# Kernel tuning notes

Hardware: AMD Instinct MI355X
Metric: run time of the kernel (lower is better)

The kernel has to match this reference:

```python
import jax, jax.numpy as jnp
import numpy as np


def _conv1x1(x, w, b):
    # x: (B,Ci,H,W), w: (Co,Ci) -> (B,Co,H,W)
    return jnp.einsum('bchw,oc->bohw', x, w) + b[None, :, None, None]


def _conv3x3(x, w, b):
    # x: (B,Ci,H,W), w: (Co,Ci,3,3), stride 1, padding 1 ('SAME')
    y = jax.lax.conv_general_dilated(
        x, w, window_strides=(1, 1), padding='SAME',
        dimension_numbers=('NCHW', 'OIHW', 'NCHW'))
    return y + b[None, :, None, None]


def setup_inputs() -> dict:
    key = jax.random.key(0)
    ks = jax.random.split(key, 10)
    N, B, Cc, Cf, H, W = 3, 8, 128, 256, 64, 64
    s = 0.05  # weight scale to keep attention logits well-conditioned
    return {
        'contexts': jax.random.normal(ks[0], (N, B, Cc, 2 * H, 2 * W), jnp.float32),
        'mainstream': jax.random.normal(ks[1], (B, Cf, H, W), jnp.float32),
        'Wc_w': jax.random.normal(ks[2], (Cc, Cc), jnp.float32) * s,
        'Wc_b': jax.random.normal(ks[3], (Cc,), jnp.float32) * s,
        'Wf_w': jax.random.normal(ks[4], (Cc, Cf), jnp.float32) * s,
        'Wf_b': jax.random.normal(ks[5], (Cc,), jnp.float32) * s,
        'Wk_w': jax.random.normal(ks[6], (Cc, Cf), jnp.float32) * s,
        'Wk_b': jax.random.normal(ks[7], (Cc,), jnp.float32) * s,
        'Wv_w': jax.random.normal(ks[8], (Cc, Cf, 3, 3), jnp.float32) * s,
        'Wv_b': jax.random.normal(ks[9], (Cc,), jnp.float32) * s,
    }


def reference(contexts, mainstream, Wc_w, Wc_b, Wf_w, Wf_b, Wk_w, Wk_b, Wv_w, Wv_b):
    N, B, Cc = contexts.shape[0], contexts.shape[1], contexts.shape[2]
    H, W = mainstream.shape[2], mainstream.shape[3]

    q = _conv1x1(mainstream, Wf_w, Wf_b)        # (B,Cc,H,W) queries
    mkey = _conv1x1(mainstream, Wk_w, Wk_b)     # (B,Cc,H,W) mainline keys
    vals = _conv3x3(mainstream, Wv_w, Wv_b)     # (B,Cc,H,W) mainline values
    ckeys = jax.vmap(lambda c: _conv1x1(c, Wc_w, Wc_b))(contexts)  # (N,B,Cc,2H,2W)

    # unfold 2x2 sub-pixel blocks: (.., 2H, 2W) -> (.., H, 2, W, 2)
    ckeys = ckeys.reshape(N, B, Cc, H, 2, W, 2)
    cfeat = contexts.reshape(N, B, Cc, H, 2, W, 2)

    # per-pixel cross-attention logits: context keys . query
    logits_ctx = jnp.einsum('nbchiwj,bchw->nbhiwj', ckeys, q)      # (N,B,H,2,W,2)
    # mainline key . query (same logit for all 4 sub-pixels)
    logit_main = jnp.einsum('bchw,bchw->bhw', mkey, q)[None, :, :, None, :, None]
    logits = jnp.concatenate(
        [logits_ctx, jnp.broadcast_to(logit_main, (1, B, H, 2, W, 2))], axis=0)

    attn = jax.nn.softmax(logits, axis=0)                          # (N+1,B,H,2,W,2)

    vfeat = jnp.broadcast_to(vals[None, :, :, :, None, :, None],
                             (1, B, Cc, H, 2, W, 2))
    feats = jnp.concatenate([cfeat, vfeat], axis=0)                # (N+1,B,Cc,H,2,W,2)

    out = jnp.einsum('nbhiwj,nbchiwj->bchiwj', attn, feats)        # (B,Cc,H,2,W,2)
    return out.reshape(B, Cc, 2 * H, 2 * W)
```

## Files before the change

### kernel.cpp

```cpp
#include <hip/hip_runtime.h>

#define NCTX 3
#define B 8
#define CC 128
#define CF 256
#define H 64
#define W 64
#define HW 4096
#define YX 16384

#define WS_QT    0
#define WS_VALS  4194304
#define WS_BIAS  8388608
#define WS_LM    8421376
#define WS_WALL  8454144
#define WS_MSP   8552960
#define WS_WB    13013504
#define WS_WALLO 13160960

typedef __attribute__((ext_vector_type(8))) short bf16x8;
typedef __attribute__((ext_vector_type(4))) float f32x4;
typedef __attribute__((ext_vector_type(8))) unsigned short u16x8;

__device__ __forceinline__ unsigned short f2b(float f) {
    union { float f; unsigned u; } c; c.f = f;
    unsigned u = c.u + 0x7FFFu + ((c.u >> 16) & 1u);
    return (unsigned short)(u >> 16);
}
__device__ __forceinline__ float b2f(unsigned short u) {
    union { unsigned u; float f; } c; c.u = ((unsigned)u) << 16;
    return c.f;
}

__global__ void k0(const float* __restrict__ Wc_w, const float* __restrict__ Wc_b,
                   const float* __restrict__ Wf_w, const float* __restrict__ Wf_b,
                   const float* __restrict__ Wk_w, const float* __restrict__ Wk_b,
                   const float* __restrict__ Wv,
                   unsigned short* __restrict__ Wall, unsigned short* __restrict__ Wallo,
                   float* __restrict__ bias448, unsigned short* __restrict__ Wb,
                   unsigned short* __restrict__ msP) {
    int blk = blockIdx.x;
    int t = threadIdx.x;
    if (blk < 448) {
        int o = blk * 256 + t;
        int ci8 = o & 7;
        int idx = o >> 3;
        int row = idx % 448;
        int sc4 = idx / 448;
        int f = (sc4 >> 2) * 32 + (sc4 & 3) * 8 + ci8;
        float w;
        if (row < 128) {
            float s = 0.f;
            for (int o2 = 0; o2 < 128; ++o2) s += Wc_w[o2 * 128 + row] * Wf_w[o2 * 256 + f];
            w = s;
        } else if (row < 384) {
            int p = (row - 128) >> 1;
            w = (row & 1) ? Wk_w[p * 256 + f] : Wf_w[p * 256 + f];
        } else if (row == 384) {
            float s = 0.f;
            for (int o2 = 0; o2 < 128; ++o2) s += Wc_b[o2] * Wf_w[o2 * 256 + f];
            w = s;
        } else w = 0.f;
        unsigned short hi = f2b(w);
        Wall[o] = hi;
        Wallo[o] = f2b(w - b2f(hi));
        if (o < 448) {
            float bb;
            if (o < 128) {
                float s = 0.f;
                for (int o2 = 0; o2 < 128; ++o2) s += Wc_w[o2 * 128 + o] * Wf_b[o2];
                bb = s;
            } else if (o < 384) {
                int p = (o - 128) >> 1;
                bb = (o & 1) ? Wk_b[p] : Wf_b[p];
            } else if (o == 384) {
                float s = 0.f;
                for (int o2 = 0; o2 < 128; ++o2) s += Wc_b[o2] * Wf_b[o2];
                bb = s;
            } else if (o == 385) bb = -1.f;
            else bb = 0.f;
            bias448[o] = bb;
        }
    } else if (blk < 1600) {
        int o = (blk - 448) * 256 + t;
        int ci8 = o & 7;
        int co  = (o >> 3) & 127;
        int c4  = (o >> 10) & 3;
        int s   = (o >> 12) & 7;
        int khw = o >> 15;
        int ci  = s * 32 + c4 * 8 + ci8;
        int kh  = khw / 3, kw = khw - kh * 3;
        Wb[o] = f2b(Wv[((co * 256 + ci) * 3 + kh) * 3 + kw]);
    } else {
        int i = (blk - 1600) * 256 + t;
        if (i < 66560) {
            size_t off;
            if (i < 33792) {
                int x = i % 66; int r = i / 66;
                int g = r & 31, rowi = (r >> 5) & 1, b = r >> 6;
                off = ((((size_t)b * 66 + rowi * 65) * 32) + g) * 66 + x;
            } else {
                int k = i - 33792;
                int xi = k & 1; int g = (k >> 1) & 31; int y1 = (k >> 6) & 63; int b = k >> 12;
                off = ((((size_t)b * 66 + (y1 + 1)) * 32) + g) * 66 + xi * 65;
            }
            *(u16x8*)&msP[off * 8] = (u16x8){0, 0, 0, 0, 0, 0, 0, 0};
        }
    }
}

__global__ __launch_bounds__(256) void k2p(const float* __restrict__ ms,
                                           unsigned short* __restrict__ msP,
                                           unsigned short* __restrict__ msLo) {
    __shared__ float Ls[32][65];
    int t = threadIdx.x;
    int blk = blockIdx.x;
    int s = blk & 7;
    int h = (blk >> 3) & 63;
    int b = blk >> 9;
    const float* src = ms + ((size_t)b * 256 + s * 32) * HW + h * 64;
    for (int l = t; l < 2048; l += 256) {
        int ci = l >> 6, w = l & 63;
        Ls[ci][w] = src[ci * HW + w];
    }
    __syncthreads();
    int w = t & 63, gi = t >> 6;
    u16x8 vh, vl;
#pragma unroll
    for (int j = 0; j < 8; ++j) {
        float f = Ls[gi * 8 + j][w];
        unsigned short hb = f2b(f);
        vh[j] = hb;
        vl[j] = f2b(f - b2f(hb));
    }
    size_t offH = ((((size_t)b * 66 + (h + 1)) * 32) + (s * 4 + gi)) * 66 + (w + 1);
    *(u16x8*)&msP[offH * 8] = vh;
    size_t offL = ((((size_t)b * 64 + h) * 32) + (s * 4 + gi)) * 64 + w;
    *(u16x8*)&msLo[offL * 8] = vl;
}

__global__ __launch_bounds__(512, 4) void k1m(const unsigned short* __restrict__ msP,
                                              const unsigned short* __restrict__ msLo,
                                              const unsigned short* __restrict__ Wall,
                                              const unsigned short* __restrict__ Wallo,
                                              const float* __restrict__ bias448,
                                              float* __restrict__ qt, float* __restrict__ lm) {
    __shared__ unsigned short Bs[2][2][4][64][8];
    __shared__ float biasS[448];
    __shared__ float lmAcc[64];
    int t = threadIdx.x;
    int lane = t & 63, wid = t >> 6;
    int wm = wid >> 1, wn = wid & 1;
    int b = blockIdx.x >> 6, h = blockIdx.x & 63;
    int c4l = lane >> 4, lrow = lane & 15;
    for (int i = t; i < 448; i += 512) biasS[i] = bias448[i];
    if (t < 64) lmAcc[t] = 0.f;

    f32x4 acc[7][2];
#pragma unroll
    for (int mf = 0; mf < 7; ++mf)
#pragma unroll
        for (int nf = 0; nf < 2; ++nf) acc[mf][nf] = (f32x4){0.f, 0.f, 0.f, 0.f};

    const bf16x8* Whip = (const bf16x8*)Wall;
    const bf16x8* Wlop = (const bf16x8*)Wallo;

#define STAGE1(bufv, sv) do {                                                       \
    int pl_ = wid >> 2, c4_ = wid & 3;                                              \
    if (pl_ == 0) {                                                                 \
        const unsigned short* gph = msP +                                           \
            (((((size_t)b * 66 + (h + 1)) * 32) + ((sv) * 4 + c4_)) * 66            \
             + (lane + 1)) * 8;                                                     \
        __builtin_amdgcn_global_load_lds(                                           \
            (const __attribute__((address_space(1))) void*)gph,                     \
            (__attribute__((address_space(3))) void*)&Bs[bufv][0][c4_][0][0],       \
            16, 0, 0);                                                              \
    } else {                                                                        \
        const unsigned short* gpl = msLo +                                          \
            (((((size_t)b * 64 + h) * 32) + ((sv) * 4 + c4_)) * 64 + lane) * 8;     \
        __builtin_amdgcn_global_load_lds(                                           \
            (const __attribute__((address_space(1))) void*)gpl,                     \
            (__attribute__((address_space(3))) void*)&Bs[bufv][1][c4_][0][0],       \
            16, 0, 0);                                                              \
    }                                                                               \
} while (0)

    STAGE1(0, 0);
    __syncthreads();

    for (int s = 0; s < 8; ++s) {
        int cur = s & 1;
        if (s < 7) STAGE1(cur ^ 1, s + 1);
        bf16x8 bh[2], bl[2];
#pragma unroll
        for (int nf = 0; nf < 2; ++nf) {
            int x = wn * 32 + nf * 16 + lrow;
            bh[nf] = *(const bf16x8*)&Bs[cur][0][c4l][x][0];
            bl[nf] = *(const bf16x8*)&Bs[cur][1][c4l][x][0];
        }
#pragma unroll
        for (int mf = 0; mf < 7; ++mf) {
            size_t widx = (size_t)(s * 4 + c4l) * 448 + wm * 112 + mf * 16 + lrow;
            bf16x8 ah = Whip[widx];
            bf16x8 al = Wlop[widx];
#pragma unroll
            for (int nf = 0; nf < 2; ++nf) {
                acc[mf][nf] = __builtin_amdgcn_mfma_f32_16x16x32_bf16(ah, bh[nf], acc[mf][nf], 0, 0, 0);
                acc[mf][nf] = __builtin_amdgcn_mfma_f32_16x16x32_bf16(ah, bl[nf], acc[mf][nf], 0, 0, 0);
                acc[mf][nf] = __builtin_amdgcn_mfma_f32_16x16x32_bf16(al, bh[nf], acc[mf][nf], 0, 0, 0);
            }
        }
        __syncthreads();
    }

    int px0 = wn * 32;
    float lmp[2] = {0.f, 0.f};
#pragma unroll
    for (int mf = 0; mf < 7; ++mf) {
        int base = wm * 112 + mf * 16;
        int r0 = base + c4l * 4;
        if (base < 128) {
#pragma unroll
            for (int nf = 0; nf < 2; ++nf) {
                int x = px0 + nf * 16 + lrow;
                float* dst = qt + ((size_t)b * 128 + r0) * HW + h * 64 + x;
                f32x4 v = acc[mf][nf];
#pragma unroll
                for (int j = 0; j < 4; ++j)
                    dst[(size_t)j * HW] = v[j] + biasS[r0 + j];
            }
        } else {
            float b0 = biasS[r0], b1 = biasS[r0 + 1], b2 = biasS[r0 + 2], b3 = biasS[r0 + 3];
#pragma unroll
            for (int nf = 0; nf < 2; ++nf) {
                f32x4 v = acc[mf][nf];
                lmp[nf] += (v[0] + b0) * (v[1] + b1) + (v[2] + b2) * (v[3] + b3);
            }
        }
    }
    if (wm != 0) {
#pragma unroll
        for (int nf = 0; nf < 2; ++nf) {
            lmp[nf] += __shfl_xor(lmp[nf], 16);
            lmp[nf] += __shfl_xor(lmp[nf], 32);
        }
        if (c4l == 0) {
#pragma unroll
            for (int nf = 0; nf < 2; ++nf)
                atomicAdd(&lmAcc[px0 + nf * 16 + lrow], lmp[nf]);
        }
    }
    __syncthreads();
    if (t < 64) lm[b * HW + h * 64 + t] = lmAcc[t];
#undef STAGE1
}

__global__ __launch_bounds__(256, 4) void k2m(const unsigned short* __restrict__ msP,
                                              const unsigned short* __restrict__ Wb,
                                              const float* __restrict__ Wv_b,
                                              float* __restrict__ vals) {
    __shared__ unsigned short Bs[2][6336];
    __shared__ float biasS[128];
    int t = threadIdx.x;
    int lane = t & 63, wid = t >> 6;
    int wm = wid;
    int b = blockIdx.x >> 6, h = blockIdx.x & 63;
    int c4l = lane >> 4, lrow = lane & 15;
    if (t < 128) biasS[t] = Wv_b[t];

    f32x4 acc[2][4];
#pragma unroll
    for (int mf = 0; mf < 2; ++mf)
#pragma unroll
        for (int nf = 0; nf < 4; ++nf) acc[mf][nf] = (f32x4){0.f, 0.f, 0.f, 0.f};

    const bf16x8* Wbp = (const bf16x8*)Wb;

#define STAGE(bufv, sv) do {                                                        \
    for (int iter = 0; iter < 4; ++iter) {                                          \
        int q0 = iter * 256 + (wid << 6);                                           \
        int q = q0 + lane;                                                          \
        if (q < 792) {                                                              \
            int rc = q / 66; int x = q - rc * 66;                                   \
            int r = rc >> 2, c4 = rc & 3;                                           \
            int y = h + r;                                   \
            const unsigned short* gp = msP +                                        \
                (((((size_t)b * 66 + y) * 32) + ((sv) * 4 + c4)) * 66 + x) * 8;     \
            unsigned short* lp = &Bs[bufv][q0 * 8];                                 \
            __builtin_amdgcn_global_load_lds(                                       \
                (const __attribute__((address_space(1))) void*)gp,                  \
                (__attribute__((address_space(3))) void*)lp, 16, 0, 0);             \
        }                                                                           \
    }                                                                               \
} while (0)

    STAGE(0, 0);
    __syncthreads();

    for (int s = 0; s < 8; ++s) {
        int cur = s & 1;
        if (s < 7) STAGE(cur ^ 1, s + 1);
#pragma unroll
        for (int khw = 0; khw < 9; ++khw) {
            int kh = khw / 3, kw = khw - 3 * (khw / 3);
            bf16x8 a[2];
#pragma unroll
            for (int mf = 0; mf < 2; ++mf)
                a[mf] = Wbp[((khw * 8 + s) * 4 + c4l) * 128 + wm * 32 + mf * 16 + lrow];
            bf16x8 bf[4];
#pragma unroll
            for (int nf = 0; nf < 4; ++nf) {
                int chunk = (kh * 4 + c4l) * 66 + nf * 16 + lrow + kw;
                bf[nf] = *(const bf16x8*)&Bs[cur][chunk * 8];
            }
#pragma unroll
            for (int mf = 0; mf < 2; ++mf)
#pragma unroll
                for (int nf = 0; nf < 4; ++nf)
                    acc[mf][nf] = __builtin_amdgcn_mfma_f32_16x16x32_bf16(
                        a[mf], bf[nf], acc[mf][nf], 0, 0, 0);
        }
        __syncthreads();
    }

#pragma unroll
    for (int mf = 0; mf < 2; ++mf) {
        int co0 = wm * 32 + mf * 16 + c4l * 4;
#pragma unroll
        for (int nf = 0; nf < 4; ++nf) {
            int x = nf * 16 + lrow;
            float* dst = vals + (((size_t)b * 128 + co0) * HW) + h * 64 + x;
            f32x4 v = acc[mf][nf];
#pragma unroll
            for (int j = 0; j < 4; ++j)
                dst[(size_t)j * HW] = v[j] + biasS[co0 + j];
        }
    }
#undef STAGE
}

__global__ __launch_bounds__(256, 2) void k3(
    const float* __restrict__ ctx, const float* __restrict__ qt,
    const float* __restrict__ vals, const float* __restrict__ lm,
    float* __restrict__ out) {
    __shared__ float part[4][3][64];
    __shared__ float attnS[4][64];
    int t = threadIdx.x;
    int lane = t & 63, wv = t >> 6;
    int xg = t & 15, cq = t >> 4;
    int blk = blockIdx.x;
    int b = blk >> 8, y = (blk >> 1) & 127, xh = blk & 1;
    int h = y >> 1;
    int x0 = xh * 64 + xg * 4;
    int p0 = xh * 32 + xg * 2;

    float2 qv[8], vv[8];
    const float* qbase = qt + ((size_t)b * 128 + cq * 8) * HW + h * 64 + p0;
    const float* vbase = vals + ((size_t)b * 128 + cq * 8) * HW + h * 64 + p0;
#pragma unroll
    for (int j = 0; j < 8; ++j) {
        qv[j] = *(const float2*)&qbase[(size_t)j * HW];
        vv[j] = *(const float2*)&vbase[(size_t)j * HW];
    }
    float4 cx[3][8];
#pragma unroll
    for (int n = 0; n < 3; ++n) {
        const float* cb = ctx + ((size_t)(n * 8 + b) * 128 + cq * 8) * YX + (size_t)y * 128 + x0;
#pragma unroll
        for (int j = 0; j < 8; ++j) cx[n][j] = *(const float4*)&cb[(size_t)j * YX];
    }
    float lp[3][4];
#pragma unroll
    for (int n = 0; n < 3; ++n) {
#pragma unroll
        for (int xl = 0; xl < 4; ++xl) lp[n][xl] = 0.f;
#pragma unroll
        for (int j = 0; j < 8; ++j) {
            lp[n][0] += cx[n][j].x * qv[j].x;
            lp[n][1] += cx[n][j].y * qv[j].x;
            lp[n][2] += cx[n][j].z * qv[j].y;
            lp[n][3] += cx[n][j].w * qv[j].y;
        }
    }
#pragma unroll
    for (int n = 0; n < 3; ++n)
#pragma unroll
        for (int xl = 0; xl < 4; ++xl) {
            float v = lp[n][xl];
            v += __shfl_xor(v, 16);
            v += __shfl_xor(v, 32);
            lp[n][xl] = v;
        }
    if (lane < 16) {
#pragma unroll
        for (int n = 0; n < 3; ++n)
#pragma unroll
            for (int xl = 0; xl < 4; ++xl)
                part[wv][n][lane * 4 + xl] = lp[n][xl];
    }
    __syncthreads();
    if (t < 64) {
        float l0 = part[0][0][t] + part[1][0][t] + part[2][0][t] + part[3][0][t];
        float l1 = part[0][1][t] + part[1][1][t] + part[2][1][t] + part[3][1][t];
        float l2 = part[0][2][t] + part[1][2][t] + part[2][2][t] + part[3][2][t];
        float l3 = lm[(size_t)b * HW + h * 64 + xh * 32 + (t >> 1)];
        float m = fmaxf(fmaxf(l0, l1), fmaxf(l2, l3));
        float e0 = __expf(l0 - m), e1 = __expf(l1 - m), e2 = __expf(l2 - m), e3 = __expf(l3 - m);
        float inv = 1.f / (e0 + e1 + e2 + e3);
        attnS[0][t] = e0 * inv; attnS[1][t] = e1 * inv;
        attnS[2][t] = e2 * inv; attnS[3][t] = e3 * inv;
    }
    __syncthreads();
    float a0[4], a1[4], a2[4], a3[4];
#pragma unroll
    for (int xl = 0; xl < 4; ++xl) {
        a0[xl] = attnS[0][xg * 4 + xl];
        a1[xl] = attnS[1][xg * 4 + xl];
        a2[xl] = attnS[2][xg * 4 + xl];
        a3[xl] = attnS[3][xg * 4 + xl];
    }
    float* obase = out + ((size_t)b * 128 + cq * 8) * YX + (size_t)y * 128 + x0;
#pragma unroll
    for (int j = 0; j < 8; ++j) {
        float4 o;
        o.x = a3[0] * vv[j].x + a0[0] * cx[0][j].x + a1[0] * cx[1][j].x + a2[0] * cx[2][j].x;
        o.y = a3[1] * vv[j].x + a0[1] * cx[0][j].y + a1[1] * cx[1][j].y + a2[1] * cx[2][j].y;
        o.z = a3[2] * vv[j].y + a0[2] * cx[0][j].z + a1[2] * cx[1][j].z + a2[2] * cx[2][j].z;
        o.w = a3[3] * vv[j].y + a0[3] * cx[0][j].w + a1[3] * cx[1][j].w + a2[3] * cx[2][j].w;
        *(float4*)&obase[(size_t)j * YX] = o;
    }
}

extern "C" void kernel_launch(void* const* d_in, const int* in_sizes, int n_in,
                              void* d_out, int out_size, void* d_ws, size_t ws_size,
                              hipStream_t stream) {
    const float* ctx  = (const float*)d_in[0];
    const float* ms   = (const float*)d_in[1];
    const float* Wc_w = (const float*)d_in[2];
    const float* Wc_b = (const float*)d_in[3];
    const float* Wf_w = (const float*)d_in[4];
    const float* Wf_b = (const float*)d_in[5];
    const float* Wk_w = (const float*)d_in[6];
    const float* Wk_b = (const float*)d_in[7];
    const float* Wv_w = (const float*)d_in[8];
    const float* Wv_b = (const float*)d_in[9];
    float* out = (float*)d_out;
    float* ws = (float*)d_ws;
    float* qt      = ws + WS_QT;
    float* vals    = ws + WS_VALS;
    float* bias448 = ws + WS_BIAS;
    float* lmp     = ws + WS_LM;
    unsigned short* Wallp  = (unsigned short*)(ws + WS_WALL);
    unsigned short* Wallop = (unsigned short*)(ws + WS_WALLO);
    unsigned short* msPp   = (unsigned short*)(ws + WS_MSP);
    unsigned short* msLop  = (unsigned short*)(ws + WS_VALS);
    unsigned short* Wbp    = (unsigned short*)(ws + WS_WB);

    hipLaunchKernelGGL(k0, dim3(1860), dim3(256), 0, stream, Wc_w, Wc_b, Wf_w, Wf_b,
                       Wk_w, Wk_b, Wv_w, Wallp, Wallop, bias448, Wbp, msPp);
    hipLaunchKernelGGL(k2p, dim3(4096), dim3(256), 0, stream, ms, msPp, msLop);
    hipLaunchKernelGGL(k1m, dim3(512), dim3(512), 0, stream, msPp, msLop, Wallp, Wallop,
                       bias448, qt, lmp);
    hipLaunchKernelGGL(k2m, dim3(512), dim3(256), 0, stream, msPp, Wbp, Wv_b, vals);
    hipLaunchKernelGGL(k3, dim3(2048), dim3(256), 0, stream, ctx, qt, vals, lmp, out);
}
```

Before: 153.4 us.

## Merge prep into k0 and fuse 1x1 and 3x3 GEMM kernels into one launch

Folds the bf16 packing of mainstream into the weight-prep kernel as extra blocks, so one launch does both. The 1x1 GEMM now reads fp32 mainstream directly and does the hi/lo bf16 split in registers while prefetching the next stage, which drops the separate low-part buffer and its global round trip. The 1x1 and 3x3 conv GEMMs are merged into one launch of 1024 blocks, 512 per branch, with the 3x3 branch moved to 512 threads and a swizzled row order. This saves two launches and lets the two GEMMs overlap on the device. The cost is a lower-bandwidth strided fp32 load path and conversion work inside the GEMM loop.

```diff
diff --git a/kernel.cpp b/kernel.cpp
--- a/kernel.cpp
+++ b/kernel.cpp
@@ -32,13 +32,15 @@
     return c.f;
 }
 
-__global__ void k0(const float* __restrict__ Wc_w, const float* __restrict__ Wc_b,
-                   const float* __restrict__ Wf_w, const float* __restrict__ Wf_b,
-                   const float* __restrict__ Wk_w, const float* __restrict__ Wk_b,
-                   const float* __restrict__ Wv,
-                   unsigned short* __restrict__ Wall, unsigned short* __restrict__ Wallo,
-                   float* __restrict__ bias448, unsigned short* __restrict__ Wb,
-                   unsigned short* __restrict__ msP) {
+__global__ __launch_bounds__(256) void k0(
+    const float* __restrict__ Wc_w, const float* __restrict__ Wc_b,
+    const float* __restrict__ Wf_w, const float* __restrict__ Wf_b,
+    const float* __restrict__ Wk_w, const float* __restrict__ Wk_b,
+    const float* __restrict__ Wv, const float* __restrict__ ms,
+    unsigned short* __restrict__ Wall, unsigned short* __restrict__ Wallo,
+    float* __restrict__ bias448, unsigned short* __restrict__ Wb,
+    unsigned short* __restrict__ msP) {
+    __shared__ float Ls[32][65];
     int blk = blockIdx.x;
     int t = threadIdx.x;
     if (blk < 448) {
@@ -91,7 +93,7 @@
         int ci  = s * 32 + c4 * 8 + ci8;
         int kh  = khw / 3, kw = khw - kh * 3;
         Wb[o] = f2b(Wv[((co * 256 + ci) * 3 + kh) * 3 + kw]);
-    } else {
+    } else if (blk < 1860) {
         int i = (blk - 1600) * 256 + t;
         if (i < 66560) {
             size_t off;
@@ -106,237 +108,228 @@
             }
             *(u16x8*)&msP[off * 8] = (u16x8){0, 0, 0, 0, 0, 0, 0, 0};
         }
-    }
-}
-
-__global__ __launch_bounds__(256) void k2p(const float* __restrict__ ms,
-                                           unsigned short* __restrict__ msP,
-                                           unsigned short* __restrict__ msLo) {
-    __shared__ float Ls[32][65];
-    int t = threadIdx.x;
-    int blk = blockIdx.x;
-    int s = blk & 7;
-    int h = (blk >> 3) & 63;
-    int b = blk >> 9;
-    const float* src = ms + ((size_t)b * 256 + s * 32) * HW + h * 64;
-    for (int l = t; l < 2048; l += 256) {
-        int ci = l >> 6, w = l & 63;
-        Ls[ci][w] = src[ci * HW + w];
-    }
-    __syncthreads();
-    int w = t & 63, gi = t >> 6;
-    u16x8 vh, vl;
-#pragma unroll
-    for (int j = 0; j < 8; ++j) {
-        float f = Ls[gi * 8 + j][w];
-        unsigned short hb = f2b(f);
-        vh[j] = hb;
-        vl[j] = f2b(f - b2f(hb));
-    }
-    size_t offH = ((((size_t)b * 66 + (h + 1)) * 32) + (s * 4 + gi)) * 66 + (w + 1);
-    *(u16x8*)&msP[offH * 8] = vh;
-    size_t offL = ((((size_t)b * 64 + h) * 32) + (s * 4 + gi)) * 64 + w;
-    *(u16x8*)&msLo[offL * 8] = vl;
-}
-
-__global__ __launch_bounds__(512, 4) void k1m(const unsigned short* __restrict__ msP,
-                                              const unsigned short* __restrict__ msLo,
-                                              const unsigned short* __restrict__ Wall,
-                                              const unsigned short* __restrict__ Wallo,
-                                              const float* __restrict__ bias448,
-                                              float* __restrict__ qt, float* __restrict__ lm) {
-    __shared__ unsigned short Bs[2][2][4][64][8];
-    __shared__ float biasS[448];
-    __shared__ float lmAcc[64];
+    } else {
+        int local = blk - 1860;
+        int s = local & 7;
+        int h = (local >> 3) & 63;
+        int b = local >> 9;
+        const float* src = ms + ((size_t)b * 256 + s * 32) * HW + h * 64;
+        for (int l = t; l < 2048; l += 256) {
+            int ci = l >> 6, w = l & 63;
+            Ls[ci][w] = src[ci * HW + w];
+        }
+        __syncthreads();
+        int w = t & 63, gi = t >> 6;
+        u16x8 vh;
+#pragma unroll
+        for (int j = 0; j < 8; ++j) vh[j] = f2b(Ls[gi * 8 + j][w]);
+        size_t offH = ((((size_t)b * 66 + (h + 1)) * 32) + (s * 4 + gi)) * 66 + (w + 1);
+        *(u16x8*)&msP[offH * 8] = vh;
+    }
+}
+
+__global__ __launch_bounds__(512, 4) void kmm(
+    const float* __restrict__ ms, const unsigned short* __restrict__ msP,
+    const unsigned short* __restrict__ Wall, const unsigned short* __restrict__ Wallo,
+    const float* __restrict__ bias448, const unsigned short* __restrict__ Wb,
+    const float* __restrict__ Wv_b,
+    float* __restrict__ qt, float* __restrict__ lm, float* __restrict__ vals) {
+    __shared__ unsigned char smem[25856] __attribute__((aligned(16)));
     int t = threadIdx.x;
     int lane = t & 63, wid = t >> 6;
-    int wm = wid >> 1, wn = wid & 1;
-    int b = blockIdx.x >> 6, h = blockIdx.x & 63;
     int c4l = lane >> 4, lrow = lane & 15;
-    for (int i = t; i < 448; i += 512) biasS[i] = bias448[i];
-    if (t < 64) lmAcc[t] = 0.f;
-
-    f32x4 acc[7][2];
-#pragma unroll
-    for (int mf = 0; mf < 7; ++mf)
-#pragma unroll
-        for (int nf = 0; nf < 2; ++nf) acc[mf][nf] = (f32x4){0.f, 0.f, 0.f, 0.f};
-
-    const bf16x8* Whip = (const bf16x8*)Wall;
-    const bf16x8* Wlop = (const bf16x8*)Wallo;
-
-#define STAGE1(bufv, sv) do {                                                       \
-    int pl_ = wid >> 2, c4_ = wid & 3;                                              \
-    if (pl_ == 0) {                                                                 \
-        const unsigned short* gph = msP +                                           \
-            (((((size_t)b * 66 + (h + 1)) * 32) + ((sv) * 4 + c4_)) * 66            \
-             + (lane + 1)) * 8;                                                     \
-        __builtin_amdgcn_global_load_lds(                                           \
-            (const __attribute__((address_space(1))) void*)gph,                     \
-            (__attribute__((address_space(3))) void*)&Bs[bufv][0][c4_][0][0],       \
-            16, 0, 0);                                                              \
-    } else {                                                                        \
-        const unsigned short* gpl = msLo +                                          \
-            (((((size_t)b * 64 + h) * 32) + ((sv) * 4 + c4_)) * 64 + lane) * 8;     \
-        __builtin_amdgcn_global_load_lds(                                           \
-            (const __attribute__((address_space(1))) void*)gpl,                     \
-            (__attribute__((address_space(3))) void*)&Bs[bufv][1][c4_][0][0],       \
-            16, 0, 0);                                                              \
-    }                                                                               \
-} while (0)
-
-    STAGE1(0, 0);
-    __syncthreads();
-
-    for (int s = 0; s < 8; ++s) {
-        int cur = s & 1;
-        if (s < 7) STAGE1(cur ^ 1, s + 1);
-        bf16x8 bh[2], bl[2];
-#pragma unroll
-        for (int nf = 0; nf < 2; ++nf) {
-            int x = wn * 32 + nf * 16 + lrow;
-            bh[nf] = *(const bf16x8*)&Bs[cur][0][c4l][x][0];
-            bl[nf] = *(const bf16x8*)&Bs[cur][1][c4l][x][0];
-        }
+    int blk = blockIdx.x;
+
+    if (blk < 512) {
+        auto Bs = (unsigned short (*)[2][4][64][8])smem;
+        float* biasS = (float*)(smem + 16384);
+        float* lmAcc = (float*)(smem + 16384 + 1792);
+        int wm = wid >> 1, wn = wid & 1;
+        int b = blk >> 6, h = blk & 63;
+        int xs = t & 63, g4 = t >> 6;
+        int c4w = g4 >> 1, sub = g4 & 1;
+        const float* msb = ms + ((size_t)b * 256 + g4 * 4) * HW + h * 64 + xs;
+        for (int i = t; i < 448; i += 512) biasS[i] = bias448[i];
+        if (t < 64) lmAcc[t] = 0.f;
+
+        f32x4 acc[7][2];
+#pragma unroll
+        for (int mf = 0; mf < 7; ++mf)
+#pragma unroll
+            for (int nf = 0; nf < 2; ++nf) acc[mf][nf] = (f32x4){0.f, 0.f, 0.f, 0.f};
+
+        const bf16x8* Whip = (const bf16x8*)Wall;
+        const bf16x8* Wlop = (const bf16x8*)Wallo;
+
+#define CVT_WRITE(bufv, F0, F1, F2, F3) do {                                    \
+        unsigned short h0 = f2b(F0), h1 = f2b(F1), h2 = f2b(F2), h3 = f2b(F3);  \
+        unsigned short q0 = f2b((F0) - b2f(h0)), q1 = f2b((F1) - b2f(h1));      \
+        unsigned short q2 = f2b((F2) - b2f(h2)), q3 = f2b((F3) - b2f(h3));      \
+        uint2 hw, lw;                                                           \
+        hw.x = (unsigned)h0 | ((unsigned)h1 << 16);                             \
+        hw.y = (unsigned)h2 | ((unsigned)h3 << 16);                             \
+        lw.x = (unsigned)q0 | ((unsigned)q1 << 16);                             \
+        lw.y = (unsigned)q2 | ((unsigned)q3 << 16);                             \
+        *(uint2*)&Bs[bufv][0][c4w][xs][sub * 4] = hw;                           \
+        *(uint2*)&Bs[bufv][1][c4w][xs][sub * 4] = lw;                           \
+    } while (0)
+
+        {
+            float f0 = msb[0], f1 = msb[HW], f2 = msb[2 * HW], f3 = msb[3 * HW];
+            CVT_WRITE(0, f0, f1, f2, f3);
+        }
+        __syncthreads();
+
+        for (int s = 0; s < 8; ++s) {
+            int cur = s & 1;
+            float fn0, fn1, fn2, fn3;
+            if (s < 7) {
+                const float* p = msb + (size_t)(s + 1) * 32 * HW;
+                fn0 = p[0]; fn1 = p[HW]; fn2 = p[2 * HW]; fn3 = p[3 * HW];
+            }
+            bf16x8 bh[2], bl[2];
+#pragma unroll
+            for (int nf = 0; nf < 2; ++nf) {
+                int x = wn * 32 + nf * 16 + lrow;
+                bh[nf] = *(const bf16x8*)&Bs[cur][0][c4l][x][0];
+                bl[nf] = *(const bf16x8*)&Bs[cur][1][c4l][x][0];
+            }
+#pragma unroll
+            for (int mf = 0; mf < 7; ++mf) {
+                size_t widx = (size_t)(s * 4 + c4l) * 448 + wm * 112 + mf * 16 + lrow;
+                bf16x8 ah = Whip[widx];
+                bf16x8 al = Wlop[widx];
+#pragma unroll
+                for (int nf = 0; nf < 2; ++nf) {
+                    acc[mf][nf] = __builtin_amdgcn_mfma_f32_16x16x32_bf16(ah, bh[nf], acc[mf][nf], 0, 0, 0);
+                    acc[mf][nf] = __builtin_amdgcn_mfma_f32_16x16x32_bf16(ah, bl[nf], acc[mf][nf], 0, 0, 0);
+                    acc[mf][nf] = __builtin_amdgcn_mfma_f32_16x16x32_bf16(al, bh[nf], acc[mf][nf], 0, 0, 0);
+                }
+            }
+            if (s < 7) CVT_WRITE(cur ^ 1, fn0, fn1, fn2, fn3);
+            __syncthreads();
+        }
+#undef CVT_WRITE
+
+        int px0 = wn * 32;
+        float lmp[2] = {0.f, 0.f};
 #pragma unroll
         for (int mf = 0; mf < 7; ++mf) {
-            size_t widx = (size_t)(s * 4 + c4l) * 448 + wm * 112 + mf * 16 + lrow;
-            bf16x8 ah = Whip[widx];
-            bf16x8 al = Wlop[widx];
+            int base = wm * 112 + mf * 16;
+            int r0 = base + c4l * 4;
+            if (base < 128) {
+#pragma unroll
+                for (int nf = 0; nf < 2; ++nf) {
+                    int x = px0 + nf * 16 + lrow;
+                    float* dst = qt + ((size_t)b * 128 + r0) * HW + h * 64 + x;
+                    f32x4 v = acc[mf][nf];
+#pragma unroll
+                    for (int j = 0; j < 4; ++j)
+                        dst[(size_t)j * HW] = v[j] + biasS[r0 + j];
+                }
+            } else {
+                float b0 = biasS[r0], b1 = biasS[r0 + 1], b2 = biasS[r0 + 2], b3 = biasS[r0 + 3];
+#pragma unroll
+                for (int nf = 0; nf < 2; ++nf) {
+                    f32x4 v = acc[mf][nf];
+                    lmp[nf] += (v[0] + b0) * (v[1] + b1) + (v[2] + b2) * (v[3] + b3);
+                }
+            }
+        }
+        if (wm != 0) {
 #pragma unroll
             for (int nf = 0; nf < 2; ++nf) {
-                acc[mf][nf] = __builtin_amdgcn_mfma_f32_16x16x32_bf16(ah, bh[nf], acc[mf][nf], 0, 0, 0);
-                acc[mf][nf] = __builtin_amdgcn_mfma_f32_16x16x32_bf16(ah, bl[nf], acc[mf][nf], 0, 0, 0);
-                acc[mf][nf] = __builtin_amdgcn_mfma_f32_16x16x32_bf16(al, bh[nf], acc[mf][nf], 0, 0, 0);
+                lmp[nf] += __shfl_xor(lmp[nf], 16);
+                lmp[nf] += __shfl_xor(lmp[nf], 32);
+            }
+            if (c4l == 0) {
+#pragma unroll
+                for (int nf = 0; nf < 2; ++nf)
+                    atomicAdd(&lmAcc[px0 + nf * 16 + lrow], lmp[nf]);
             }
         }
         __syncthreads();
-    }
-
-    int px0 = wn * 32;
-    float lmp[2] = {0.f, 0.f};
-#pragma unroll
-    for (int mf = 0; mf < 7; ++mf) {
-        int base = wm * 112 + mf * 16;
-        int r0 = base + c4l * 4;
-        if (base < 128) {
+        if (t < 64) lm[b * HW + h * 64 + t] = lmAcc[t];
+    } else {
+        auto Bs = (unsigned short (*)[6336])smem;
+        float* biasS = (float*)(smem + 25344);
+        int local = blk - 512;
+        int b = local >> 6;
+        int hl = local & 63;
+        int h = ((hl & 7) << 3) | (hl >> 3);
+        int wm = wid >> 1, wn = wid & 1;
+        if (t < 128) biasS[t] = Wv_b[t];
+
+        f32x4 acc[2][2];
+#pragma unroll
+        for (int mf = 0; mf < 2; ++mf)
+#pragma unroll
+            for (int nf = 0; nf < 2; ++nf) acc[mf][nf] = (f32x4){0.f, 0.f, 0.f, 0.f};
+
+        const bf16x8* Wbp = (const bf16x8*)Wb;
+
+#define STAGE2(bufv, sv) do {                                                       \
+        for (int iter = 0; iter < 2; ++iter) {                                      \
+            int q0 = iter * 512 + (wid << 6);                                       \
+            int q = q0 + lane;                                                      \
+            if (q < 792) {                                                          \
+                int rc = q / 66; int x = q - rc * 66;                               \
+                int r = rc >> 2, c4 = rc & 3;                                       \
+                int y = h + r;                               \
+                const unsigned short* gp = msP +                                    \
+                    (((((size_t)b * 66 + y) * 32) + ((sv) * 4 + c4)) * 66 + x) * 8; \
+                unsigned short* lp = &Bs[bufv][q0 * 8];                             \
+                __builtin_amdgcn_global_load_lds(                                   \
+                    (const __attribute__((address_space(1))) void*)gp,              \
+                    (__attribute__((address_space(3))) void*)lp, 16, 0, 0);         \
+            }                                                                       \
+        }                                                                           \
+    } while (0)
+
+        STAGE2(0, 0);
+        __syncthreads();
+
+        for (int s = 0; s < 8; ++s) {
+            int cur = s & 1;
+            if (s < 7) STAGE2(cur ^ 1, s + 1);
+#pragma unroll
+            for (int khw = 0; khw < 9; ++khw) {
+                int kh = khw / 3, kw = khw - 3 * (khw / 3);
+                bf16x8 a[2];
+#pragma unroll
+                for (int mf = 0; mf < 2; ++mf)
+                    a[mf] = Wbp[((khw * 8 + s) * 4 + c4l) * 128 + wm * 32 + mf * 16 + lrow];
+                bf16x8 bf[2];
+#pragma unroll
+                for (int nf = 0; nf < 2; ++nf) {
+                    int chunk = (kh * 4 + c4l) * 66 + wn * 32 + nf * 16 + lrow + kw;
+                    bf[nf] = *(const bf16x8*)&Bs[cur][chunk * 8];
+                }
+#pragma unroll
+                for (int mf = 0; mf < 2; ++mf)
+#pragma unroll
+                    for (int nf = 0; nf < 2; ++nf)
+                        acc[mf][nf] = __builtin_amdgcn_mfma_f32_16x16x32_bf16(
+                            a[mf], bf[nf], acc[mf][nf], 0, 0, 0);
+            }
+            __syncthreads();
+        }
+#undef STAGE2
+
+#pragma unroll
+        for (int mf = 0; mf < 2; ++mf) {
+            int co0 = wm * 32 + mf * 16 + c4l * 4;
 #pragma unroll
             for (int nf = 0; nf < 2; ++nf) {
-                int x = px0 + nf * 16 + lrow;
-                float* dst = qt + ((size_t)b * 128 + r0) * HW + h * 64 + x;
+                int x = wn * 32 + nf * 16 + lrow;
+                float* dst = vals + (((size_t)b * 128 + co0) * HW) + h * 64 + x;
                 f32x4 v = acc[mf][nf];
 #pragma unroll
                 for (int j = 0; j < 4; ++j)
-                    dst[(size_t)j * HW] = v[j] + biasS[r0 + j];
-            }
-        } else {
-            float b0 = biasS[r0], b1 = biasS[r0 + 1], b2 = biasS[r0 + 2], b3 = biasS[r0 + 3];
-#pragma unroll
-            for (int nf = 0; nf < 2; ++nf) {
-                f32x4 v = acc[mf][nf];
-                lmp[nf] += (v[0] + b0) * (v[1] + b1) + (v[2] + b2) * (v[3] + b3);
-            }
-        }
-    }
-    if (wm != 0) {
-#pragma unroll
-        for (int nf = 0; nf < 2; ++nf) {
-            lmp[nf] += __shfl_xor(lmp[nf], 16);
-            lmp[nf] += __shfl_xor(lmp[nf], 32);
-        }
-        if (c4l == 0) {
-#pragma unroll
-            for (int nf = 0; nf < 2; ++nf)
-                atomicAdd(&lmAcc[px0 + nf * 16 + lrow], lmp[nf]);
-        }
-    }
-    __syncthreads();
-    if (t < 64) lm[b * HW + h * 64 + t] = lmAcc[t];
-#undef STAGE1
-}
-
-__global__ __launch_bounds__(256, 4) void k2m(const unsigned short* __restrict__ msP,
-                                              const unsigned short* __restrict__ Wb,
-                                              const float* __restrict__ Wv_b,
-                                              float* __restrict__ vals) {
-    __shared__ unsigned short Bs[2][6336];
-    __shared__ float biasS[128];
-    int t = threadIdx.x;
-    int lane = t & 63, wid = t >> 6;
-    int wm = wid;
-    int b = blockIdx.x >> 6, h = blockIdx.x & 63;
-    int c4l = lane >> 4, lrow = lane & 15;
-    if (t < 128) biasS[t] = Wv_b[t];
-
-    f32x4 acc[2][4];
-#pragma unroll
-    for (int mf = 0; mf < 2; ++mf)
-#pragma unroll
-        for (int nf = 0; nf < 4; ++nf) acc[mf][nf] = (f32x4){0.f, 0.f, 0.f, 0.f};
-
-    const bf16x8* Wbp = (const bf16x8*)Wb;
-
-#define STAGE(bufv, sv) do {                                                        \
-    for (int iter = 0; iter < 4; ++iter) {                                          \
-        int q0 = iter * 256 + (wid << 6);                                           \
-        int q = q0 + lane;                                                          \
-        if (q < 792) {                                                              \
-            int rc = q / 66; int x = q - rc * 66;                                   \
-            int r = rc >> 2, c4 = rc & 3;                                           \
-            int y = h + r;                                   \
-            const unsigned short* gp = msP +                                        \
-                (((((size_t)b * 66 + y) * 32) + ((sv) * 4 + c4)) * 66 + x) * 8;     \
-            unsigned short* lp = &Bs[bufv][q0 * 8];                                 \
-            __builtin_amdgcn_global_load_lds(                                       \
-                (const __attribute__((address_space(1))) void*)gp,                  \
-                (__attribute__((address_space(3))) void*)lp, 16, 0, 0);             \
-        }                                                                           \
-    }                                                                               \
-} while (0)
-
-    STAGE(0, 0);
-    __syncthreads();
-
-    for (int s = 0; s < 8; ++s) {
-        int cur = s & 1;
-        if (s < 7) STAGE(cur ^ 1, s + 1);
-#pragma unroll
-        for (int khw = 0; khw < 9; ++khw) {
-            int kh = khw / 3, kw = khw - 3 * (khw / 3);
-            bf16x8 a[2];
-#pragma unroll
-            for (int mf = 0; mf < 2; ++mf)
-                a[mf] = Wbp[((khw * 8 + s) * 4 + c4l) * 128 + wm * 32 + mf * 16 + lrow];
-            bf16x8 bf[4];
-#pragma unroll
-            for (int nf = 0; nf < 4; ++nf) {
-                int chunk = (kh * 4 + c4l) * 66 + nf * 16 + lrow + kw;
-                bf[nf] = *(const bf16x8*)&Bs[cur][chunk * 8];
-            }
-#pragma unroll
-            for (int mf = 0; mf < 2; ++mf)
-#pragma unroll
-                for (int nf = 0; nf < 4; ++nf)
-                    acc[mf][nf] = __builtin_amdgcn_mfma_f32_16x16x32_bf16(
-                        a[mf], bf[nf], acc[mf][nf], 0, 0, 0);
-        }
-        __syncthreads();
-    }
-
-#pragma unroll
-    for (int mf = 0; mf < 2; ++mf) {
-        int co0 = wm * 32 + mf * 16 + c4l * 4;
-#pragma unroll
-        for (int nf = 0; nf < 4; ++nf) {
-            int x = nf * 16 + lrow;
-            float* dst = vals + (((size_t)b * 128 + co0) * HW) + h * 64 + x;
-            f32x4 v = acc[mf][nf];
-#pragma unroll
-            for (int j = 0; j < 4; ++j)
-                dst[(size_t)j * HW] = v[j] + biasS[co0 + j];
-        }
-    }
-#undef STAGE
+                    dst[(size_t)j * HW] = v[j] + biasS[co0 + j];
+            }
+        }
+    }
 }
 
 __global__ __launch_bounds__(256, 2) void k3(
@@ -453,14 +446,11 @@
     unsigned short* Wallp  = (unsigned short*)(ws + WS_WALL);
     unsigned short* Wallop = (unsigned short*)(ws + WS_WALLO);
     unsigned short* msPp   = (unsigned short*)(ws + WS_MSP);
-    unsigned short* msLop  = (unsigned short*)(ws + WS_VALS);
     unsigned short* Wbp    = (unsigned short*)(ws + WS_WB);
 
-    hipLaunchKernelGGL(k0, dim3(1860), dim3(256), 0, stream, Wc_w, Wc_b, Wf_w, Wf_b,
-                       Wk_w, Wk_b, Wv_w, Wallp, Wallop, bias448, Wbp, msPp);
-    hipLaunchKernelGGL(k2p, dim3(4096), dim3(256), 0, stream, ms, msPp, msLop);
-    hipLaunchKernelGGL(k1m, dim3(512), dim3(512), 0, stream, msPp, msLop, Wallp, Wallop,
-                       bias448, qt, lmp);
-    hipLaunchKernelGGL(k2m, dim3(512), dim3(256), 0, stream, msPp, Wbp, Wv_b, vals);
+    hipLaunchKernelGGL(k0, dim3(5956), dim3(256), 0, stream, Wc_w, Wc_b, Wf_w, Wf_b,
+                       Wk_w, Wk_b, Wv_w, ms, Wallp, Wallop, bias448, Wbp, msPp);
+    hipLaunchKernelGGL(kmm, dim3(1024), dim3(512), 0, stream, ms, msPp, Wallp, Wallop,
+                       bias448, Wbp, Wv_b, qt, lmp, vals);
     hipLaunchKernelGGL(k3, dim3(2048), dim3(256), 0, stream, ctx, qt, vals, lmp, out);
 }
```

Result: faster. 146.3 us (-4.6%).
